# Kernel optimization log

Hardware: AMD Instinct MI355X
Metric: run time of the kernel (lower is better)

## Reference

```python
import jax, jax.numpy as jnp
import numpy as np

N_FILTERS = 64
FILTER_SIZE = 64
N_FRAMES = 64
N_TO_KEEP = 128
MIN_SIZE = 512
N_SAMPLES = 32768
BATCH = 8


def pos_encoding(n_elements, n_sinusoids):
    t = np.linspace(1e-8, 1.0, n_elements)
    freq = np.linspace(1e-3, 1.0, n_sinusoids)
    return np.sin(t[:, None] * freq[None, :]).astype(np.float32)


def gammatone_filter_bank(n_filters, size, sr=22050.0):
    # 4th-order gammatone impulse responses, linearly spaced center freqs
    t = np.arange(size) / sr
    freqs = np.linspace(20.0, sr / 2 - 20.0, n_filters)
    b = 1.019 * 24.7 * (4.37 * freqs / 1000.0 + 1.0)  # ERB bandwidths
    g = (t[None, :] ** 3) * np.exp(-2 * np.pi * b[:, None] * t[None, :]) \
        * np.cos(2 * np.pi * freqs[:, None] * t[None, :])
    g = g / (np.abs(g).max(axis=-1, keepdims=True) + 1e-12)
    return g.astype(np.float32)


def setup_inputs() -> dict:
    key = jax.random.key(0)
    k1, k2 = jax.random.split(key)
    return {
        'target': jax.random.normal(k1, (BATCH, 1, N_SAMPLES), dtype=jnp.float32),
        'recon': jax.random.normal(k2, (BATCH, 1, N_SAMPLES), dtype=jnp.float32),
        'filters': jnp.asarray(gammatone_filter_bank(N_FILTERS, FILTER_SIZE)),
        'proj_time': jnp.asarray(pos_encoding(N_FRAMES, 128)),
        'proj_freq': jnp.asarray(pos_encoding(N_FILTERS, 128)),
    }


def fft_frequency_decompose(x, min_size):
    # band-limited octave decomposition: band of size s holds rfft bins [s/4, s/2)
    coeffs = jnp.fft.rfft(x, norm='ortho')
    n = x.shape[-1]
    bands = []
    start, end = 0, min_size // 2
    while end <= n // 2:
        spec = jnp.zeros(x.shape[:-1] + (end + 1,), dtype=coeffs.dtype)
        spec = spec.at[..., start:end].set(coeffs[..., start:end])
        bands.append(jnp.fft.irfft(spec, n=end * 2, norm='ortho'))
        start, end = end, end * 2
    return bands


def fft_convolve(a, b):
    n = a.shape[-1]
    pa = jnp.pad(a, [(0, 0)] * (a.ndim - 1) + [(0, n)])
    pb = jnp.pad(b, [(0, 0)] * (b.ndim - 1) + [(0, n)])
    spec = jnp.fft.rfft(pa) * jnp.fft.rfft(pb)  # broadcasts [B,1,.] x [1,F,.]
    return jnp.fft.irfft(spec, n=2 * n)[..., :n]


def max_pool1d(x, kernel, stride, pad):
    return jax.lax.reduce_window(
        x, -jnp.inf, jax.lax.max,
        (1, 1, kernel), (1, 1, stride),
        [(0, 0), (0, 0), (pad, pad)])


def sparsify2(x, k):
    # top-k over flattened (channels*time); pack events as value-scaled time
    # one-hots and binary channel one-hots
    b, c, t = x.shape
    flat = x.reshape(b, c * t)
    values, indices = jax.lax.top_k(flat, k)  # [b, k]
    ch, tm = indices // t, indices % t
    packed = (tm[..., None] == jnp.arange(t)[None, None, :]).astype(x.dtype) * values[..., None]  # [b,k,t]
    one_hot = (ch[..., None] == jnp.arange(c)[None, None, :]).astype(x.dtype)  # [b,k,c]
    return packed, one_hot


def _feature(x, filters, proj_time, proj_freq):
    bands = fft_frequency_decompose(x, MIN_SIZE)
    outs = []
    for band in bands:  # fixed small set of structurally distinct bands
        samples = band.shape[-1]
        filt = jnp.pad(filters[None, :, :], ((0, 0), (0, 0), (0, samples - FILTER_SIZE)))
        result = fft_convolve(band, filt)  # [B, n_filters, samples]
        stride = samples // 64
        pooled = max_pool1d(result, 2 * stride, stride, stride // 2)[..., :samples]  # [B, 64, 64]
        packed, one_hot = sparsify2(pooled, N_TO_KEEP)
        a = packed @ proj_time   # [B, k, 128]
        b = one_hot @ proj_freq  # [B, k, 128]
        outs.append(jnp.concatenate([a, b], axis=-1))
    return jnp.concatenate(outs, axis=-1)  # [B, k, 256 * n_bands]


def reference(target, recon, filters, proj_time, proj_freq):
    t = _feature(target, filters, proj_time, proj_freq)
    r = _feature(recon, filters, proj_time, proj_freq)
    return jnp.abs(t - r).mean()
```

## Files before the change

### kernel.cpp

```cpp
#include <hip/hip_runtime.h>
#include <hip/hip_bf16.h>

#define N_SAMP    32768
#define NBINS     16384
#define NSIG      16
#define NBANDS    7
#define K_TOP     128
#define BAND_STRIDE 65472

#define SST_F   0
#define SST_PT  4096
#define SST_PF  12288
#define SST_TOT 20480

#define TWO_PI 6.283185307179586f

typedef __attribute__((ext_vector_type(8))) short bf16x8;
typedef __attribute__((ext_vector_type(4))) float f32x4;

__device__ __forceinline__ float bf2f(__hip_bfloat16 v) { return __bfloat162float(v); }

__device__ __forceinline__ unsigned encf(float f) {
    unsigned u = __float_as_uint(f);
    return (u & 0x80000000u) ? ~u : (u | 0x80000000u);
}
__device__ __forceinline__ float decf(unsigned u) {
    return __uint_as_float((u & 0x80000000u) ? (u ^ 0x80000000u) : ~u);
}

__device__ __forceinline__ int band_M1sh(int b) { return b < 3 ? 4 : (b < 4 ? 5 : 6); }
__device__ __forceinline__ int band_Lsh(int b) {
    return b == 0 ? 5 : (b == 1 ? 6 : (b < 5 ? 7 : (b == 5 ? 8 : 9)));
}
__device__ __forceinline__ int band_M2sh(int b) {
    return b < 2 ? 4 : (b < 5 ? 5 : (b == 5 ? 6 : 7));
}

__global__ __launch_bounds__(256) void k_stage(
    const void* __restrict__ t, const void* __restrict__ f,
    const void* __restrict__ pt, const void* __restrict__ pf,
    __hip_bfloat16* __restrict__ staged,
    float* __restrict__ bands, float* __restrict__ accum,
    int* __restrict__ counter)
{
    const int tid = threadIdx.x;
    const int bx  = blockIdx.x;
    if (bx == SST_TOT / 256) {
        for (int i = tid; i < NSIG * 448; i += 256) {
            int sig = i / 448, rem = i - sig * 448;
            int g = rem >> 6, j = rem & 63;
            int off = 64 * g + 512 * ((1 << g) - 1);
            bands[(size_t)sig * BAND_STRIDE + off + j] = 0.f;
        }
        if (tid == 0) { accum[0] = 0.f; counter[0] = 0; }
        return;
    }
    float pv = bf2f(((const __hip_bfloat16*)t)[tid & 63]);
    int bad = (fabsf(pv) > 1e8f) || (pv != pv);
    const int isf32 = (__ballot(bad) != 0ull);
    const int id = bx * 256 + tid;
    const void* src; int idx;
    if (id < SST_PT)      { src = f;  idx = id; }
    else if (id < SST_PF) { src = pt; idx = id - SST_PT; }
    else                  { src = pf; idx = id - SST_PF; }
    float v = isf32 ? ((const float*)src)[idx]
                    : bf2f(((const __hip_bfloat16*)src)[idx]);
    staged[id] = __float2bfloat16(v);
}

__global__ __launch_bounds__(256) void k_fwd1(
    const void* __restrict__ tgt, const void* __restrict__ rec,
    float* __restrict__ T)
{
    const int tid   = threadIdx.x;
    const int sig   = blockIdx.y;
    const int nbase = (blockIdx.x & 1) * 128;
    const int kgrp  = (blockIdx.x >> 1) * 64;
    __shared__ __align__(16) __hip_bfloat16 xT[128][136];
    __shared__ float ct[128], st[128];

    if (tid < 128) {
        float sv, cv;
        sincosf(TWO_PI * (float)tid * (1.f / 128.f), &sv, &cv);
        ct[tid] = cv; st[tid] = sv;
    }

    float pv = bf2f(((const __hip_bfloat16*)tgt)[tid & 63]);
    int bad = (fabsf(pv) > 1e8f) || (pv != pv);
    const int isf32 = (__ballot(bad) != 0ull);
    const void* xsrc = (sig < 8) ? tgt : rec;
    const int soff = (sig & 7) * N_SAMP;

    const int rloc = tid & 127;
    const int chb  = (tid >> 7) * 64;
    for (int c8 = 0; c8 < 64; c8 += 8) {
        union { bf16x8 v; __hip_bfloat16 h[8]; } u;
        #pragma unroll
        for (int uu = 0; uu < 8; ++uu) {
            int n1 = chb + c8 + uu;
            int gi = soff + n1 * 256 + nbase + rloc;
            float xv = isf32 ? ((const float*)xsrc)[gi]
                             : bf2f(((const __hip_bfloat16*)xsrc)[gi]);
            u.h[uu] = __float2bfloat16(xv);
        }
        *(bf16x8*)(&xT[rloc][chb + c8]) = u.v;
    }
    __syncthreads();

    const int tl = tid & 15, quad = (tid >> 4) & 3, w = tid >> 6;
    const int k1 = kgrp + w * 16 + tl;
    bf16x8 Arh[4], Arl[4], Aih[4], Ail[4];
    #pragma unroll
    for (int ki = 0; ki < 4; ++ki) {
        union { bf16x8 v; __hip_bfloat16 h[8]; } rh, rl, ih, il;
        #pragma unroll
        for (int j = 0; j < 8; ++j) {
            int n1 = ki * 32 + quad * 8 + j;
            int tt = (k1 * n1) & 127;
            float wre = ct[tt], wim = -st[tt];
            __hip_bfloat16 h1 = __float2bfloat16(wre);
            rh.h[j] = h1;
            rl.h[j] = __float2bfloat16(wre - bf2f(h1));
            __hip_bfloat16 h2 = __float2bfloat16(wim);
            ih.h[j] = h2;
            il.h[j] = __float2bfloat16(wim - bf2f(h2));
        }
        Arh[ki] = rh.v; Arl[ki] = rl.v; Aih[ki] = ih.v; Ail[ki] = il.v;
    }

    float2* To = (float2*)T + (size_t)sig * 128 * 256;
    const int mk = kgrp + w * 16 + quad * 4;
    for (int ni = 0; ni < 8; ++ni) {
        bf16x8 B[4];
        #pragma unroll
        for (int ki = 0; ki < 4; ++ki)
            B[ki] = *(const bf16x8*)(&xT[ni * 16 + tl][ki * 32 + quad * 8]);
        f32x4 aR = {0.f,0.f,0.f,0.f}, aI = {0.f,0.f,0.f,0.f};
        #pragma unroll
        for (int ki = 0; ki < 4; ++ki) {
            aR = __builtin_amdgcn_mfma_f32_16x16x32_bf16(Arh[ki], B[ki], aR, 0, 0, 0);
            aR = __builtin_amdgcn_mfma_f32_16x16x32_bf16(Arl[ki], B[ki], aR, 0, 0, 0);
            aI = __builtin_amdgcn_mfma_f32_16x16x32_bf16(Aih[ki], B[ki], aI, 0, 0, 0);
            aI = __builtin_amdgcn_mfma_f32_16x16x32_bf16(Ail[ki], B[ki], aI, 0, 0, 0);
        }
        const int n2 = nbase + ni * 16 + tl;
        #pragma unroll
        for (int rg = 0; rg < 4; ++rg) {
            int k1e = mk + rg;
            float sv, cv;
            sincosf((TWO_PI / 32768.f) * (float)(k1e * n2), &sv, &cv);
            float Tr = aR[rg] * cv + aI[rg] * sv;
            float Ti = aI[rg] * cv - aR[rg] * sv;
            To[(size_t)k1e * 256 + n2] = make_float2(Tr, Ti);
        }
    }
}

__global__ __launch_bounds__(128) void k_fwd2(
    const float* __restrict__ T, float* __restrict__ C)
{
    const int k2  = threadIdx.x;
    const int k1  = blockIdx.x;
    const int sig = blockIdx.y;
    __shared__ float2 Ts[256];
    const float2* Tin = (const float2*)T + ((size_t)sig * 128 + k1) * 256;
    for (int i = k2; i < 256; i += 128) Ts[i] = Tin[i];
    __syncthreads();
    float er[4], ei[4];
    #pragma unroll
    for (int c = 0; c < 4; ++c) {
        float sv, cv;
        sincosf(-TWO_PI * (float)((c * k2) & 255) * (1.f / 256.f), &sv, &cv);
        er[c] = cv; ei[c] = sv;
    }
    float s4, c4;
    sincosf(-TWO_PI * (float)((4 * k2) & 255) * (1.f / 256.f), &s4, &c4);
    float Xr[4] = {0.f,0.f,0.f,0.f}, Xi[4] = {0.f,0.f,0.f,0.f};
    for (int n2 = 0; n2 < 256; n2 += 4) {
        #pragma unroll
        for (int c = 0; c < 4; ++c) {
            float2 t = Ts[n2 + c];
            Xr[c] += t.x * er[c] - t.y * ei[c];
            Xi[c] += t.x * ei[c] + t.y * er[c];
            float nr = er[c] * c4 - ei[c] * s4;
            ei[c]    = er[c] * s4 + ei[c] * c4;
            er[c] = nr;
        }
    }
    const float inv = 5.5242717280199030e-3f;
    float xr = (Xr[0] + Xr[1]) + (Xr[2] + Xr[3]);
    float xi = (Xi[0] + Xi[1]) + (Xi[2] + Xi[3]);
    float2* Co = (float2*)C + (size_t)sig * NBINS;
    Co[k1 + 128 * k2] = make_float2(xr * inv, xi * inv);
}

__global__ __launch_bounds__(256) void k_synthA(
    const float* __restrict__ C, float* __restrict__ G)
{
    const int tid = threadIdx.x;
    const int sig = blockIdx.y;
    const int bix = 63 - blockIdx.x;
    const int band = (bix == 0) ? 0 : (32 - __clz(bix));
    const int lbx  = (band == 0) ? 0 : (bix - (1 << (band - 1)));
    const int s    = 512 << band;
    const int m1sh = band_M1sh(band);
    const int lsh  = band_Lsh(band);
    const int m2sh = band_M2sh(band);
    const int M2   = 1 << m2sh;
    const int L    = 1 << lsh;
    const int L4   = L >> 2;
    const int a    = (band == 0) ? 0 : (128 << band);
    const int tix  = lbx * 256 + tid;
    const int j1lo = (lbx * 256) >> (lsh - 2);
    int j1cnt = 256 >> (lsh - 2);
    if (j1cnt > (1 << m1sh)) j1cnt = 1 << m1sh;
    __shared__ float2 Ds[256];
    const float2* D = (const float2*)C + (size_t)sig * NBINS + a;
    for (int i = tid; i < (j1cnt << m2sh); i += 256) {
        int j1o = i >> m2sh, j2 = i & (M2 - 1);
        Ds[i] = D[(j1lo + j1o) + (j2 << m1sh)];
    }
    __syncthreads();
    if (tix >= (128 << band)) return;
    const int j1o = (tix >> (lsh - 2)) - j1lo;
    const int m   = tix & (L4 - 1);
    const float2* Dj = Ds + (j1o << m2sh);
    float e0r = 1.f, e0i = 0.f, e1r, e1i, sr, si;
    sincosf(TWO_PI * (float)m / (float)L, &e1i, &e1r);
    sincosf(TWO_PI * (float)(2 * m) / (float)L, &si, &sr);
    float ar[4] = {0.f,0.f,0.f,0.f}, ai[4] = {0.f,0.f,0.f,0.f};
    for (int j2 = 0; j2 < M2; j2 += 4) {
        {   float2 d = Dj[j2];
            float tr = d.x * e0r - d.y * e0i, ti = d.x * e0i + d.y * e0r;
            ar[0] += tr; ai[0] += ti; ar[1] += tr; ai[1] += ti;
            ar[2] += tr; ai[2] += ti; ar[3] += tr; ai[3] += ti;
            float nr = e0r * sr - e0i * si; e0i = e0r * si + e0i * sr; e0r = nr;
        }
        {   float2 d = Dj[j2 + 1];
            float tr = d.x * e1r - d.y * e1i, ti = d.x * e1i + d.y * e1r;
            ar[0] += tr; ai[0] += ti;
            ar[1] -= ti; ai[1] += tr;
            ar[2] -= tr; ai[2] -= ti;
            ar[3] += ti; ai[3] -= tr;
            float nr = e1r * sr - e1i * si; e1i = e1r * si + e1i * sr; e1r = nr;
        }
        {   float2 d = Dj[j2 + 2];
            float tr = d.x * e0r - d.y * e0i, ti = d.x * e0i + d.y * e0r;
            ar[0] += tr; ai[0] += ti;
            ar[1] -= tr; ai[1] -= ti;
            ar[2] += tr; ai[2] += ti;
            ar[3] -= tr; ai[3] -= ti;
            float nr = e0r * sr - e0i * si; e0i = e0r * si + e0i * sr; e0r = nr;
        }
        {   float2 d = Dj[j2 + 3];
            float tr = d.x * e1r - d.y * e1i, ti = d.x * e1i + d.y * e1r;
            ar[0] += tr; ai[0] += ti;
            ar[1] += ti; ai[1] -= tr;
            ar[2] -= tr; ai[2] -= ti;
            ar[3] -= ti; ai[3] += tr;
            float nr = e1r * sr - e1i * si; e1i = e1r * si + e1i * sr; e1r = nr;
        }
    }
    const float sc = 2.f * rsqrtf((float)s);
    float2* Go = (float2*)G + (size_t)sig * 65024 + 512 * ((1 << band) - 1);
    const int base = ((tix >> (lsh - 2)) << lsh) + m;
    #pragma unroll
    for (int q = 0; q < 4; ++q)
        Go[base + q * L4] = make_float2(ar[q] * sc, ai[q] * sc);
}

__global__ __launch_bounds__(256) void k_synthB(
    const float* __restrict__ C, const float* __restrict__ G,
    float* __restrict__ bands)
{
    const int tid = threadIdx.x;
    const int sig = blockIdx.y;
    const int bix = 63 - blockIdx.x;
    const int band = (bix == 0) ? 0 : (32 - __clz(bix));
    const int lbx  = (band == 0) ? 0 : (bix - (1 << (band - 1)));
    const int s    = 512 << band;
    const int M1   = 1 << band_M1sh(band);
    const int lsh  = band_Lsh(band);
    const int n    = lbx * 256 + tid;
    const int s4   = s >> 2;
    if (n >= s4) return;
    const int m    = n & ((1 << lsh) - 1);
    const float2* Gi = (const float2*)G + (size_t)sig * 65024 + 512 * ((1 << band) - 1);
    float e0r = 1.f, e0i = 0.f, e1r, e1i, sr, si;
    sincosf(TWO_PI * (float)n / (float)s, &e1i, &e1r);
    sincosf(TWO_PI * (float)(2 * n) / (float)s, &si, &sr);
    float zr[4] = {0.f,0.f,0.f,0.f}, zi[4] = {0.f,0.f,0.f,0.f};
    for (int j1 = 0; j1 < M1; j1 += 4) {
        {   float2 g = Gi[((j1 + 0) << lsh) + m];
            float tr = g.x * e0r - g.y * e0i, ti = g.x * e0i + g.y * e0r;
            zr[0] += tr; zi[0] += ti; zr[1] += tr; zi[1] += ti;
            zr[2] += tr; zi[2] += ti; zr[3] += tr; zi[3] += ti;
            float nr = e0r * sr - e0i * si; e0i = e0r * si + e0i * sr; e0r = nr;
        }
        {   float2 g = Gi[((j1 + 1) << lsh) + m];
            float tr = g.x * e1r - g.y * e1i, ti = g.x * e1i + g.y * e1r;
            zr[0] += tr; zi[0] += ti;
            zr[1] -= ti; zi[1] += tr;
            zr[2] -= tr; zi[2] -= ti;
            zr[3] += ti; zi[3] -= tr;
            float nr = e1r * sr - e1i * si; e1i = e1r * si + e1i * sr; e1r = nr;
        }
        {   float2 g = Gi[((j1 + 2) << lsh) + m];
            float tr = g.x * e0r - g.y * e0i, ti = g.x * e0i + g.y * e0r;
            zr[0] += tr; zi[0] += ti;
            zr[1] -= tr; zi[1] -= ti;
            zr[2] += tr; zi[2] += ti;
            zr[3] -= tr; zi[3] -= ti;
            float nr = e0r * sr - e0i * si; e0i = e0r * si + e0i * sr; e0r = nr;
        }
        {   float2 g = Gi[((j1 + 3) << lsh) + m];
            float tr = g.x * e1r - g.y * e1i, ti = g.x * e1i + g.y * e1r;
            zr[0] += tr; zi[0] += ti;
            zr[1] += ti; zi[1] -= tr;
            zr[2] -= tr; zi[2] -= ti;
            zr[3] -= ti; zi[3] += tr;
            float nr = e1r * sr - e1i * si; e1i = e1r * si + e1i * sr; e1r = nr;
        }
    }
    const int poff = 64 * (band + 1) + 512 * ((1 << band) - 1);
    float* bo = bands + (size_t)sig * BAND_STRIDE + poff;
    if (band == 0) {
        const float dc = C[(size_t)sig * NBINS * 2] * 0.04419417382415922f;
        #pragma unroll
        for (int q = 0; q < 4; ++q) bo[n + q * s4] = zr[q] - dc;
    } else {
        #pragma unroll
        for (int q = 0; q < 4; ++q) {
            float val;
            switch (n & 3) {
                case 0:  val =  zr[q]; break;
                case 1:  val = -zi[q]; break;
                case 2:  val = -zr[q]; break;
                default: val =  zi[q]; break;
            }
            bo[n + q * s4] = val;
        }
    }
}

__global__ __launch_bounds__(256) void k_conv(
    const float* __restrict__ bands,
    const __hip_bfloat16* __restrict__ filters,
    float* __restrict__ segG)
{
    const int tid  = threadIdx.x;
    const int sig  = blockIdx.y;
    const int c    = blockIdx.x;
    const int band = 31 - __clz(c + 1);
    const int cidx = c + 1 - (1 << band);
    const int poff = 64 * (band + 1) + 512 * ((1 << band) - 1);
    const float* bp = bands + (size_t)sig * BAND_STRIDE + poff + cidx * 512;

    __shared__ __align__(16) __hip_bfloat16 xr[8][584];
    __shared__ float segP[64 * 4];

    for (int i = tid; i < 576; i += 256) {
        __hip_bfloat16 b = __float2bfloat16(bp[511 - i]);
        #pragma unroll
        for (int p = 0; p < 8; ++p) {
            int idx = i - p;
            if (idx >= 0) xr[p][idx] = b;
        }
    }
    __syncthreads();

    const int tl   = tid & 15;
    const int quad = (tid >> 4) & 3;
    const int wave = tid >> 6;

    bf16x8 bf0[4], bf1[4];
    #pragma unroll
    for (int ft = 0; ft < 4; ++ft) {
        const __hip_bfloat16* fp = filters + ((ft * 16 + tl) * 64 + quad * 8);
        bf0[ft] = *(const bf16x8*)(fp);
        bf1[ft] = *(const bf16x8*)(fp + 32);
    }

    int s0 = 511 - wave * 128 - tl + 8 * quad;
    const __hip_bfloat16* xp = &xr[0][0] + (s0 & 7) * 584 + (s0 & ~7);

    const int spc = 512 >> (2 + band);
    float* segO = segG + (size_t)(sig * NBANDS + band) * 64 * 128 + cidx * spc;

    const float NEG = -3.4e38f;
    float run0 = NEG, run1 = NEG, run2 = NEG, run3 = NEG;
    const int per = (band >= 2) ? (1 << (band - 2)) : 1;

    for (int it = 0; it < 8; ++it) {
        const int t0 = wave * 128 + it * 16;
        bf16x8 a0 = *(const bf16x8*)(xp);
        bf16x8 a1 = *(const bf16x8*)(xp + 32);
        xp -= 16;
        f32x4 ac0 = {0.f,0.f,0.f,0.f}, ac1 = ac0, ac2 = ac0, ac3 = ac0;
        ac0 = __builtin_amdgcn_mfma_f32_16x16x32_bf16(a0, bf0[0], ac0, 0, 0, 0);
        ac0 = __builtin_amdgcn_mfma_f32_16x16x32_bf16(a1, bf1[0], ac0, 0, 0, 0);
        ac1 = __builtin_amdgcn_mfma_f32_16x16x32_bf16(a0, bf0[1], ac1, 0, 0, 0);
        ac1 = __builtin_amdgcn_mfma_f32_16x16x32_bf16(a1, bf1[1], ac1, 0, 0, 0);
        ac2 = __builtin_amdgcn_mfma_f32_16x16x32_bf16(a0, bf0[2], ac2, 0, 0, 0);
        ac2 = __builtin_amdgcn_mfma_f32_16x16x32_bf16(a1, bf1[2], ac2, 0, 0, 0);
        ac3 = __builtin_amdgcn_mfma_f32_16x16x32_bf16(a0, bf0[3], ac3, 0, 0, 0);
        ac3 = __builtin_amdgcn_mfma_f32_16x16x32_bf16(a1, bf1[3], ac3, 0, 0, 0);
        float m0 = fmaxf(fmaxf(ac0[0], ac0[1]), fmaxf(ac0[2], ac0[3]));
        float m1 = fmaxf(fmaxf(ac1[0], ac1[1]), fmaxf(ac1[2], ac1[3]));
        float m2 = fmaxf(fmaxf(ac2[0], ac2[1]), fmaxf(ac2[2], ac2[3]));
        float m3 = fmaxf(fmaxf(ac3[0], ac3[1]), fmaxf(ac3[2], ac3[3]));
        if (band == 0) {
            int sb = (t0 >> 2) + quad;
            segO[(tl     ) * 128 + sb] = m0;
            segO[(tl + 16) * 128 + sb] = m1;
            segO[(tl + 32) * 128 + sb] = m2;
            segO[(tl + 48) * 128 + sb] = m3;
        } else if (band == 1) {
            m0 = fmaxf(m0, __shfl_xor(m0, 16));
            m1 = fmaxf(m1, __shfl_xor(m1, 16));
            m2 = fmaxf(m2, __shfl_xor(m2, 16));
            m3 = fmaxf(m3, __shfl_xor(m3, 16));
            if ((quad & 1) == 0) {
                int sb = (t0 >> 3) + (quad >> 1);
                segO[(tl     ) * 128 + sb] = m0;
                segO[(tl + 16) * 128 + sb] = m1;
                segO[(tl + 32) * 128 + sb] = m2;
                segO[(tl + 48) * 128 + sb] = m3;
            }
        } else {
            m0 = fmaxf(m0, __shfl_xor(m0, 16)); m0 = fmaxf(m0, __shfl_xor(m0, 32));
            m1 = fmaxf(m1, __shfl_xor(m1, 16)); m1 = fmaxf(m1, __shfl_xor(m1, 32));
            m2 = fmaxf(m2, __shfl_xor(m2, 16)); m2 = fmaxf(m2, __shfl_xor(m2, 32));
            m3 = fmaxf(m3, __shfl_xor(m3, 16)); m3 = fmaxf(m3, __shfl_xor(m3, 32));
            run0 = fmaxf(run0, m0); run1 = fmaxf(run1, m1);
            run2 = fmaxf(run2, m2); run3 = fmaxf(run3, m3);
            if (((it + 1) & (per - 1)) == 0) {
                int sb = t0 >> (2 + band);
                float rv = quad == 0 ? run0 : quad == 1 ? run1
                         : quad == 2 ? run2 : run3;
                segO[(tl + 16 * quad) * 128 + sb] = rv;
                run0 = NEG; run1 = NEG; run2 = NEG; run3 = NEG;
            }
        }
    }
    if (band == 6) {
        float rv = quad == 0 ? run0 : quad == 1 ? run1
                 : quad == 2 ? run2 : run3;
        segP[(tl + 16 * quad) * 4 + wave] = rv;
        __syncthreads();
        if (tid < 128) {
            int f = tid & 63, sg = tid >> 6;
            segO[f * 128 + sg] =
                fmaxf(segP[f * 4 + 2 * sg], segP[f * 4 + 2 * sg + 1]);
        }
    }
}

__global__ __launch_bounds__(256) void k_topk(
    const float* __restrict__ segG,
    float* __restrict__ topv, int* __restrict__ topi)
{
    const int tid = threadIdx.x;
    const int band = blockIdx.x, sig = blockIdx.y;
    const float* segB = segG + (size_t)(sig * NBANDS + band) * 64 * 128;

    __shared__ unsigned hist[256];
    __shared__ unsigned scan[256];
    __shared__ unsigned long long list[512];
    __shared__ int sh_B, sh_nA, sh_cnt, sh_num;

    unsigned long long kk[16];
    #pragma unroll
    for (int q = 0; q < 16; ++q) {
        int i = q * 256 + tid;
        int f = i >> 6, t = i & 63;
        const float* sg = segB + f * 128;
        float m = fmaxf(sg[2 * t], sg[2 * t + 1]);
        if (t > 0)  m = fmaxf(m, sg[2 * t - 1]);
        if (t < 63) m = fmaxf(m, sg[2 * t + 2]);
        kk[q] = ((unsigned long long)encf(m) << 32) | (unsigned)(4095 - i);
    }

    int shift = 56;
    unsigned long long prefix = 0;
    int nA = 0;
    for (int lev = 0; lev < 8; ++lev) {
        hist[tid] = 0;
        __syncthreads();
        #pragma unroll
        for (int q = 0; q < 16; ++q) {
            bool inpre = (lev == 0) || ((kk[q] >> (shift + 8)) == prefix);
            if (inpre) atomicAdd(&hist[(unsigned)((kk[q] >> shift) & 255u)], 1u);
        }
        __syncthreads();
        scan[tid] = hist[tid];
        __syncthreads();
        for (int off = 1; off < 256; off <<= 1) {
            unsigned v = scan[tid] + ((tid + off < 256) ? scan[tid + off] : 0u);
            __syncthreads();
            scan[tid] = v;
            __syncthreads();
        }
        {
            unsigned ge = (unsigned)nA + scan[tid];
            unsigned gt = (unsigned)nA + ((tid < 255) ? scan[tid + 1] : 0u);
            if (ge >= 128u && gt < 128u) {
                sh_B = tid; sh_nA = (int)gt; sh_cnt = (int)hist[tid];
            }
        }
        __syncthreads();
        prefix = (prefix << 8) | (unsigned)sh_B;
        nA = sh_nA;
        if (nA + sh_cnt <= 511 || shift == 0) break;
        shift -= 8;
        __syncthreads();
    }

    list[tid] = 0ull; list[tid + 256] = 0ull;
    if (tid == 0) sh_num = 0;
    __syncthreads();
    #pragma unroll
    for (int q = 0; q < 16; ++q) {
        if ((kk[q] >> shift) >= prefix) {
            int p = atomicAdd(&sh_num, 1);
            if (p < 512) list[p] = kk[q];
        }
    }
    __syncthreads();

    for (int k = 2; k <= 512; k <<= 1) {
        for (int j = k >> 1; j > 0; j >>= 1) {
            for (int w = tid; w < 512; w += 256) {
                int l = w ^ j;
                if (l > w) {
                    unsigned long long av = list[w], bv = list[l];
                    bool up = ((w & k) == 0);
                    if ((av > bv) == up) { list[w] = bv; list[l] = av; }
                }
            }
            __syncthreads();
        }
    }
    if (tid < K_TOP) {
        unsigned long long key = list[511 - tid];
        const size_t ob = ((size_t)sig * NBANDS + band) * K_TOP + tid;
        topv[ob] = decf((unsigned)(key >> 32));
        topi[ob] = 4095 - (int)(key & 0xFFFFFFFFu);
    }
}

__global__ __launch_bounds__(256) void k_loss(
    const float* __restrict__ topv, const int* __restrict__ topi,
    const __hip_bfloat16* __restrict__ PT, const __hip_bfloat16* __restrict__ PF,
    float* __restrict__ accum, int* __restrict__ counter,
    unsigned* __restrict__ out)
{
    const int tid = threadIdx.x;
    const int band = blockIdx.x, b = blockIdx.y;
    const size_t bt = ((size_t)b * NBANDS + band) * K_TOP;
    const size_t br = ((size_t)(8 + b) * NBANDS + band) * K_TOP;
    __shared__ float vT[128], vR[128];
    __shared__ int   iT[128], iR[128];
    if (tid < 128) { vT[tid] = topv[bt + tid]; iT[tid] = topi[bt + tid]; }
    else { int j = tid - 128; vR[j] = topv[br + j]; iR[j] = topi[br + j]; }
    __syncthreads();
    float sum = 0.f;
    if (tid < 128) {
        #pragma unroll 4
        for (int k = 0; k < K_TOP; ++k) {
            float a = vT[k] * bf2f(PT[(iT[k] & 63) * 128 + tid]);
            float c = vR[k] * bf2f(PT[(iR[k] & 63) * 128 + tid]);
            sum += fabsf(a - c);
        }
    } else {
        const int j = tid - 128;
        #pragma unroll 4
        for (int k = 0; k < K_TOP; ++k) {
            float a = bf2f(PF[(iT[k] >> 6) * 128 + j]);
            float c = bf2f(PF[(iR[k] >> 6) * 128 + j]);
            sum += fabsf(a - c);
        }
    }
    __shared__ float red[256];
    __shared__ int amLast;
    red[tid] = sum;
    __syncthreads();
    for (int ofs = 128; ofs > 0; ofs >>= 1) {
        if (tid < ofs) red[tid] += red[tid + ofs];
        __syncthreads();
    }
    if (tid == 0) {
        atomicAdd(accum, red[0]);
        __threadfence();
        amLast = (atomicAdd(counter, 1) == NBANDS * 8 - 1);
    }
    __syncthreads();
    if (!amLast) return;
    if (tid == 0) {
        __threadfence();
        float L = atomicAdd(accum, 0.f) * (1.0f / 1835008.0f);
        unsigned lu = __float_as_uint(L);
        bool isnanL = ((lu & 0x7F800000u) == 0x7F800000u) && (lu & 0x007FFFFFu);
        float code;
        if      (isnanL)           code = 500.f;
        else if (L == 0.f)         code = 400.f;
        else if (fabsf(L) < 1e-6f) code = 600.f;
        else                       code = L;
        unsigned fb = __float_as_uint(code);
        unsigned hb = (fb + 0x7FFFu + ((fb >> 16) & 1u)) >> 16;
        out[0] = (hb << 16) | hb;
    }
}

extern "C" void kernel_launch(void* const* d_in, const int* in_sizes, int n_in,
                              void* d_out, int out_size, void* d_ws, size_t ws_size,
                              hipStream_t stream)
{
    float* C      = (float*)d_ws;
    float* bands  = C + (size_t)NSIG * NBINS * 2;
    float* segG   = bands + (size_t)NSIG * BAND_STRIDE;
    float* topv   = segG + (size_t)NSIG * NBANDS * 64 * 128;
    int*   topi   = (int*)(topv + (size_t)NSIG * NBANDS * K_TOP);
    float* accum  = (float*)(topi + (size_t)NSIG * NBANDS * K_TOP);
    int*   counter= (int*)(accum + 1);
    __hip_bfloat16* staged = (__hip_bfloat16*)(accum + 4);
    float* TG = (float*)(staged + SST_TOT);
    float* T  = TG;
    float* G  = TG;

    const __hip_bfloat16* fst = staged + SST_F;
    const __hip_bfloat16* pts = staged + SST_PT;
    const __hip_bfloat16* pfs = staged + SST_PF;

    k_stage  <<<dim3(SST_TOT / 256 + 1), 256, 0, stream>>>(
                 d_in[0], d_in[2], d_in[3], d_in[4], staged, bands, accum, counter);
    k_fwd1   <<<dim3(4, NSIG),       256, 0, stream>>>(d_in[0], d_in[1], T);
    k_fwd2   <<<dim3(128, NSIG),     128, 0, stream>>>(T, C);
    k_synthA <<<dim3(64, NSIG),      256, 0, stream>>>(C, G);
    k_synthB <<<dim3(64, NSIG),      256, 0, stream>>>(C, G, bands);
    k_conv   <<<dim3(127, NSIG),     256, 0, stream>>>(bands, fst, segG);
    k_topk   <<<dim3(NBANDS, NSIG),  256, 0, stream>>>(segG, topv, topi);
    k_loss   <<<dim3(NBANDS, 8),     256, 0, stream>>>(topv, topi, pts, pfs,
                 accum, counter, (unsigned*)d_out);
}
```

Measured before the change: 207.5 us.

## Radix-4 split 256-point DFT in k_fwd2 so each thread yields four outputs

The second-stage 256-point DFT in k_fwd2 now has each thread compute four output bins (k2, k2+64, k2+128, k2+192) at once. The bins share twiddles, with only ±1/±i sign rotations between them, so complex multiplies and twiddle recurrences drop about fourfold. Blocks now handle four k1 rows with 256 threads, so there are 32 blocks per signal instead of 128. The cost is fewer, larger blocks, slightly different rounding from the changed twiddle recurrence, and scattered stores of four outputs per thread.

```diff
diff --git a/kernel.cpp b/kernel.cpp
--- a/kernel.cpp
+++ b/kernel.cpp
@@ -156,42 +156,65 @@
     }
 }
 
-__global__ __launch_bounds__(128) void k_fwd2(
+__global__ __launch_bounds__(256) void k_fwd2(
     const float* __restrict__ T, float* __restrict__ C)
 {
-    const int k2  = threadIdx.x;
-    const int k1  = blockIdx.x;
+    const int tid = threadIdx.x;
     const int sig = blockIdx.y;
-    __shared__ float2 Ts[256];
-    const float2* Tin = (const float2*)T + ((size_t)sig * 128 + k1) * 256;
-    for (int i = k2; i < 256; i += 128) Ts[i] = Tin[i];
-    __syncthreads();
-    float er[4], ei[4];
+    const int k1b = blockIdx.x * 4;
+    const int kl  = tid >> 6;
+    const int k2  = tid & 63;
+    __shared__ float2 Ts[4][256];
+    const float2* Tin = (const float2*)T + ((size_t)sig * 128 + k1b) * 256;
+    for (int i = tid; i < 1024; i += 256) Ts[i >> 8][i & 255] = Tin[i];
+    __syncthreads();
+    const float2* Tk = Ts[kl];
+    float e0r = 1.f, e0i = 0.f, e1r, e1i, sr, si;
+    sincosf(-TWO_PI * (float)k2 * (1.f / 256.f), &e1i, &e1r);
+    sincosf(-TWO_PI * (float)((2 * k2) & 255) * (1.f / 256.f), &si, &sr);
+    float Xr[4] = {0.f,0.f,0.f,0.f}, Xi[4] = {0.f,0.f,0.f,0.f};
+    for (int p = 0; p < 256; p += 4) {
+        {
+            float2 t = Tk[p];
+            float tr = t.x * e0r - t.y * e0i, ti = t.x * e0i + t.y * e0r;
+            Xr[0] += tr; Xi[0] += ti; Xr[1] += tr; Xi[1] += ti;
+            Xr[2] += tr; Xi[2] += ti; Xr[3] += tr; Xi[3] += ti;
+            float nr = e0r * sr - e0i * si; e0i = e0r * si + e0i * sr; e0r = nr;
+        }
+        {
+            float2 t = Tk[p + 1];
+            float tr = t.x * e1r - t.y * e1i, ti = t.x * e1i + t.y * e1r;
+            Xr[0] += tr; Xi[0] += ti;
+            Xr[1] += ti; Xi[1] -= tr;
+            Xr[2] -= tr; Xi[2] -= ti;
+            Xr[3] -= ti; Xi[3] += tr;
+            float nr = e1r * sr - e1i * si; e1i = e1r * si + e1i * sr; e1r = nr;
+        }
+        {
+            float2 t = Tk[p + 2];
+            float tr = t.x * e0r - t.y * e0i, ti = t.x * e0i + t.y * e0r;
+            Xr[0] += tr; Xi[0] += ti;
+            Xr[1] -= tr; Xi[1] -= ti;
+            Xr[2] += tr; Xi[2] += ti;
+            Xr[3] -= tr; Xi[3] -= ti;
+            float nr = e0r * sr - e0i * si; e0i = e0r * si + e0i * sr; e0r = nr;
+        }
+        {
+            float2 t = Tk[p + 3];
+            float tr = t.x * e1r - t.y * e1i, ti = t.x * e1i + t.y * e1r;
+            Xr[0] += tr; Xi[0] += ti;
+            Xr[1] -= ti; Xi[1] += tr;
+            Xr[2] -= tr; Xi[2] -= ti;
+            Xr[3] += ti; Xi[3] -= tr;
+            float nr = e1r * sr - e1i * si; e1i = e1r * si + e1i * sr; e1r = nr;
+        }
+    }
+    const float inv = 5.5242717280199030e-3f;
+    float2* Co = (float2*)C + (size_t)sig * NBINS;
+    const int k1 = k1b + kl;
     #pragma unroll
-    for (int c = 0; c < 4; ++c) {
-        float sv, cv;
-        sincosf(-TWO_PI * (float)((c * k2) & 255) * (1.f / 256.f), &sv, &cv);
-        er[c] = cv; ei[c] = sv;
-    }
-    float s4, c4;
-    sincosf(-TWO_PI * (float)((4 * k2) & 255) * (1.f / 256.f), &s4, &c4);
-    float Xr[4] = {0.f,0.f,0.f,0.f}, Xi[4] = {0.f,0.f,0.f,0.f};
-    for (int n2 = 0; n2 < 256; n2 += 4) {
-        #pragma unroll
-        for (int c = 0; c < 4; ++c) {
-            float2 t = Ts[n2 + c];
-            Xr[c] += t.x * er[c] - t.y * ei[c];
-            Xi[c] += t.x * ei[c] + t.y * er[c];
-            float nr = er[c] * c4 - ei[c] * s4;
-            ei[c]    = er[c] * s4 + ei[c] * c4;
-            er[c] = nr;
-        }
-    }
-    const float inv = 5.5242717280199030e-3f;
-    float xr = (Xr[0] + Xr[1]) + (Xr[2] + Xr[3]);
-    float xi = (Xi[0] + Xi[1]) + (Xi[2] + Xi[3]);
-    float2* Co = (float2*)C + (size_t)sig * NBINS;
-    Co[k1 + 128 * k2] = make_float2(xr * inv, xi * inv);
+    for (int q = 0; q < 4; ++q)
+        Co[k1 + 128 * (k2 + 64 * q)] = make_float2(Xr[q] * inv, Xi[q] * inv);
 }
 
 __global__ __launch_bounds__(256) void k_synthA(
@@ -635,7 +658,7 @@
     k_stage  <<<dim3(SST_TOT / 256 + 1), 256, 0, stream>>>(
                  d_in[0], d_in[2], d_in[3], d_in[4], staged, bands, accum, counter);
     k_fwd1   <<<dim3(4, NSIG),       256, 0, stream>>>(d_in[0], d_in[1], T);
-    k_fwd2   <<<dim3(128, NSIG),     128, 0, stream>>>(T, C);
+    k_fwd2   <<<dim3(32, NSIG),      256, 0, stream>>>(T, C);
     k_synthA <<<dim3(64, NSIG),      256, 0, stream>>>(C, G);
     k_synthB <<<dim3(64, NSIG),      256, 0, stream>>>(C, G, bands);
     k_conv   <<<dim3(127, NSIG),     256, 0, stream>>>(bands, fst, segG);
```

After: 209.6 us. Within noise of the previous version (+1.0%).
